# Optimization experiments

Measured on AMD Instinct MI355X. Metric: run time of the kernel, lower is better.

The kernel has to match this reference:

```python
import jax, jax.numpy as jnp
import numpy as np

N_NODES = 100000
N_EDGES = 1600000
DIM = 128


def setup_inputs() -> dict:
    key = jax.random.key(0)
    k_x, k_e, k_wm, k_bm, k_wu, k_bu = jax.random.split(key, 6)
    bound = 1.0 / np.sqrt(DIM)
    return {
        "x": jax.random.normal(k_x, (N_NODES, DIM), dtype=jnp.float32),
        "edge_index": jax.random.randint(k_e, (2, N_EDGES), 0, N_NODES, dtype=jnp.int64),
        "W_msg": jax.random.uniform(k_wm, (DIM, DIM), jnp.float32, -bound, bound),
        "b_msg": jax.random.uniform(k_bm, (DIM,), jnp.float32, -bound, bound),
        "W_upd": jax.random.uniform(k_wu, (DIM, DIM), jnp.float32, -bound, bound),
        "b_upd": jax.random.uniform(k_bu, (DIM,), jnp.float32, -bound, bound),
    }


def reference(x, edge_index, W_msg, b_msg, W_upd, b_upd):
    # message_net: Linear + ReLU on all nodes  [N, D]
    messages = jax.nn.relu(x @ W_msg.T + b_msg)
    src, dst = edge_index[0], edge_index[1]
    # gather by src, scatter-add by dst (index_add)  [N, D]
    aggregated = jax.ops.segment_sum(messages[src], dst, num_segments=x.shape[0])
    # update_net: Linear + ReLU, then residual
    updated = jax.nn.relu(aggregated @ W_upd.T + b_upd)
    return updated + x
```

## Files before the change

kernel.cpp:

```cpp
#include <hip/hip_runtime.h>
#include <hip/hip_bf16.h>

#define DIM 128
#define BNODES 64
#define CNODES 1024
#define NCMAX 128
#define NBMAX 2048
#define CCAP 20480
#define BCAP 2048
#define FB 16
#define CCHUNK 2048

typedef __attribute__((ext_vector_type(8))) short bf16x8;
typedef __attribute__((ext_vector_type(4))) float f32x4;

__device__ inline ushort f2bf(float f) {
    uint u = __float_as_uint(f);
    u += 0x7fffu + ((u >> 16) & 1u);
    return (ushort)(u >> 16);
}
__device__ inline uint pack2(float lo, float hi) {
    return (uint)f2bf(lo) | ((uint)f2bf(hi) << 16);
}

__device__ __forceinline__
void linear_body_bf16out(const float* in, const float* __restrict__ W,
                         const float* __restrict__ b, ushort* out,
                         int n_tiles, int bid, int nblocks, uint4* Wl)
{
    const int t = threadIdx.x;
    for (int q = t; q < 2048; q += 256) {
        const int j = q >> 4, c = q & 15;
        const float4 lo = ((const float4*)(W + j * 128 + c * 8))[0];
        const float4 hi = ((const float4*)(W + j * 128 + c * 8))[1];
        uint4 pk;
        pk.x = pack2(lo.x, lo.y); pk.y = pack2(lo.z, lo.w);
        pk.z = pack2(hi.x, hi.y); pk.w = pack2(hi.z, hi.w);
        Wl[j * 16 + (c ^ (j & 15))] = pk;
    }
    __syncthreads();

    const int lane = t & 63;
    const int lo4 = lane & 15;
    const int g   = lane >> 4;

    float bias[8];
    #pragma unroll
    for (int ct = 0; ct < 8; ++ct) bias[ct] = b[ct * 16 + lo4];

    const int wid = (bid * 256 + t) >> 6;
    const int nw  = (nblocks * 256) >> 6;

    for (int tile = wid; tile < n_tiles; tile += nw) {
        const int arow = tile * 16 + lo4;
        const float4* ap = (const float4*)(in + (size_t)arow * DIM + g * 32);
        float4 v[8];
        #pragma unroll
        for (int i = 0; i < 8; ++i) v[i] = ap[i];

        bf16x8 afrag[4];
        #pragma unroll
        for (int ks = 0; ks < 4; ++ks) {
            union { bf16x8 v8; uint u[4]; } a;
            a.u[0] = pack2(v[2*ks].x,   v[2*ks].y);
            a.u[1] = pack2(v[2*ks].z,   v[2*ks].w);
            a.u[2] = pack2(v[2*ks+1].x, v[2*ks+1].y);
            a.u[3] = pack2(v[2*ks+1].z, v[2*ks+1].w);
            afrag[ks] = a.v8;
        }

        f32x4 acc[8];
        #pragma unroll
        for (int ct = 0; ct < 8; ++ct)
            acc[ct] = (f32x4){bias[ct], bias[ct], bias[ct], bias[ct]};

        #pragma unroll
        for (int ks = 0; ks < 4; ++ks) {
            #pragma unroll
            for (int ct = 0; ct < 8; ++ct) {
                const int jrow = ct * 16 + lo4;
                const bf16x8 bfrag = *((const bf16x8*)&Wl[jrow * 16 + ((g * 4 + ks) ^ lo4)]);
                acc[ct] = __builtin_amdgcn_mfma_f32_16x16x32_bf16(afrag[ks], bfrag, acc[ct], 0, 0, 0);
            }
        }

        #pragma unroll
        for (int ct = 0; ct < 8; ++ct) {
            #pragma unroll
            for (int r = 0; r < 4; ++r) {
                const int orow = tile * 16 + g * 4 + r;
                const int ocol = ct * 16 + lo4;
                out[(size_t)orow * DIM + ocol] = f2bf(fmaxf(acc[ct][r], 0.f));
            }
        }
    }
}

__global__ __launch_bounds__(256, 2)
void lin1_coarse_kernel(const float* x, const float* __restrict__ Wm,
                        const float* __restrict__ bm, ushort* msg, int n_tiles,
                        const int* __restrict__ ei, int* __restrict__ ccur,
                        uint* __restrict__ cedges, int n_edges, int ncb, int cb)
{
    __shared__ uint4 Wl[128 * 16];

    const int bid = (int)blockIdx.x;
    bool coarse;
    int rid;
    if (bid < 2 * cb) { coarse = !(bid & 1); rid = bid >> 1; }
    else              { coarse = false;      rid = cb + (bid - 2 * cb); }

    if (coarse) {
        uint*   packedL = (uint*)Wl;
        ushort* regionL = (ushort*)(packedL + CCHUNK);
        int*    histC   = (int*)(regionL + CCHUNK);
        int*    startC  = histC + NCMAX;
        int*    gbaseC  = startC + NCMAX;
        int*    curC    = gbaseC + NCMAX;

        const int t = threadIdx.x;
        const int chunk = (n_edges + cb - 1) / cb;
        const int e0 = rid * chunk;
        const int e1 = min(e0 + chunk, n_edges);
        const int cnt = e1 - e0;

        if (t < NCMAX) histC[t] = 0;
        __syncthreads();
        for (int i = t; i < cnt; i += 256)
            atomicAdd(&histC[ei[n_edges + e0 + i] >> 10], 1);
        __syncthreads();
        if (t < NCMAX) startC[t] = histC[t];
        for (int off = 1; off < NCMAX; off <<= 1) {
            int add = 0;
            __syncthreads();
            if (t < NCMAX && t >= off) add = startC[t - off];
            __syncthreads();
            if (t < NCMAX) startC[t] += add;
        }
        __syncthreads();
        if (t < NCMAX) {
            const int excl = startC[t] - histC[t];
            startC[t] = excl;
            curC[t] = excl;
            gbaseC[t] = (t < ncb && histC[t]) ? atomicAdd(&ccur[t], histC[t]) : 0;
        }
        __syncthreads();
        for (int i = t; i < cnt; i += 256) {
            const int src = ei[e0 + i];
            const int dst = ei[n_edges + e0 + i];
            const int r = dst >> 10;
            const int pos = atomicAdd(&curC[r], 1);
            packedL[pos] = ((uint)src << 10) | (uint)(dst & 1023);
            regionL[pos] = (ushort)r;
        }
        __syncthreads();
        for (int i = t; i < cnt; i += 256) {
            const int r = regionL[i];
            const int off = gbaseC[r] + (i - startC[r]);
            if (off < CCAP)
                cedges[(size_t)r * CCAP + off] = packedL[i];
        }
    } else {
        linear_body_bf16out(x, Wm, bm, msg, n_tiles, rid,
                            (int)gridDim.x - cb, Wl);
    }
}

__global__ __launch_bounds__(256)
void fine_scatter_kernel(const int* __restrict__ ccnt, const uint* __restrict__ cedges,
                         int* __restrict__ gcur, uint* __restrict__ bedges, int ncb)
{
    __shared__ int histL[FB];
    __shared__ int curL[FB];
    const int t = threadIdx.x;
    const int c = blockIdx.x >> 3;
    const int s = blockIdx.x & 7;
    const int cnt = min(ccnt[c], CCAP);
    const int chunk = (cnt + 7) / 8;
    const int e0 = s * chunk;
    const int e1 = min(e0 + chunk, cnt);
    if (t < FB) histL[t] = 0;
    __syncthreads();
    const uint* ce = cedges + (size_t)c * CCAP;
    for (int i = e0 + t; i < e1; i += 256)
        atomicAdd(&histL[(ce[i] & 1023u) >> 6], 1);
    __syncthreads();
    if (t < FB)
        curL[t] = histL[t] ? atomicAdd(&gcur[c * FB + t], histL[t]) : 0;
    __syncthreads();
    for (int i = e0 + t; i < e1; i += 256) {
        const uint p = ce[i];
        const uint dl = p & 1023u;
        const int f = (int)(dl >> 6);
        const int pos = atomicAdd(&curL[f], 1);
        if (pos < BCAP)
            bedges[(size_t)(c * FB + f) * BCAP + pos] = ((p >> 10) << 6) | (dl & 63u);
    }
}

__global__ __launch_bounds__(512)
void bucket_gather_kernel(const uint* __restrict__ msg, const int* __restrict__ gcur,
                          const uint* __restrict__ bedges, uint* __restrict__ agg16,
                          int n_nodes)
{
    __shared__ int  srcL[BCAP];
    __shared__ int histL[BNODES];
    __shared__ int inclL[BNODES];
    __shared__ int cursL[BNODES];

    const int t = threadIdx.x;
    const int b = blockIdx.x;
    const int cnt = min(gcur[b], BCAP);
    const uint* be = bedges + (size_t)b * BCAP;

    if (t < BNODES) histL[t] = 0;
    __syncthreads();
    for (int i = t; i < cnt; i += 512)
        atomicAdd(&histL[be[i] & 63u], 1);
    __syncthreads();
    if (t < BNODES) inclL[t] = histL[t];
    for (int off = 1; off < BNODES; off <<= 1) {
        int add = 0;
        __syncthreads();
        if (t < BNODES && t >= off) add = inclL[t - off];
        __syncthreads();
        if (t < BNODES) inclL[t] += add;
    }
    __syncthreads();
    if (t < BNODES) cursL[t] = inclL[t] - histL[t];
    __syncthreads();
    for (int i = t; i < cnt; i += 512) {
        const uint p = be[i];
        const int pos = atomicAdd(&cursL[p & 63u], 1);
        srcL[pos] = (int)(p >> 6);
    }
    __syncthreads();

    const int lane = t & 63;
    const int w = t >> 6;
    for (int dl = w; dl < BNODES; dl += 8) {
        const int node = b * BNODES + dl;
        if (node >= n_nodes) break;
        const int e1 = inclL[dl];
        const int e0 = e1 - histL[dl];
        float a0 = 0.f, a1 = 0.f;
        int i = e0;
        for (; i + 8 <= e1; i += 8) {
            uint m[8];
            #pragma unroll
            for (int k = 0; k < 8; ++k)
                m[k] = msg[(size_t)srcL[i + k] * 64 + lane];
            #pragma unroll
            for (int k = 0; k < 8; ++k) {
                a0 += __uint_as_float(m[k] << 16);
                a1 += __uint_as_float(m[k] & 0xffff0000u);
            }
        }
        for (; i + 4 <= e1; i += 4) {
            uint m[4];
            #pragma unroll
            for (int k = 0; k < 4; ++k)
                m[k] = msg[(size_t)srcL[i + k] * 64 + lane];
            #pragma unroll
            for (int k = 0; k < 4; ++k) {
                a0 += __uint_as_float(m[k] << 16);
                a1 += __uint_as_float(m[k] & 0xffff0000u);
            }
        }
        for (; i < e1; ++i) {
            const uint m = msg[(size_t)srcL[i] * 64 + lane];
            a0 += __uint_as_float(m << 16);
            a1 += __uint_as_float(m & 0xffff0000u);
        }
        agg16[(size_t)node * 64 + lane] = pack2(a0, a1);
    }
}

__global__ __launch_bounds__(256, 2)
void lin2_a16_kernel(const uint4* __restrict__ agg16, const float* __restrict__ Wu,
                     const float* __restrict__ bu, const float* __restrict__ x,
                     float* __restrict__ out, int n_tiles)
{
    __shared__ uint4 Wl[128 * 16];
    const int t = threadIdx.x;
    for (int q = t; q < 2048; q += 256) {
        const int j = q >> 4, c = q & 15;
        const float4 lo = ((const float4*)(Wu + j * 128 + c * 8))[0];
        const float4 hi = ((const float4*)(Wu + j * 128 + c * 8))[1];
        uint4 pk;
        pk.x = pack2(lo.x, lo.y); pk.y = pack2(lo.z, lo.w);
        pk.z = pack2(hi.x, hi.y); pk.w = pack2(hi.z, hi.w);
        Wl[j * 16 + (c ^ (j & 15))] = pk;
    }
    __syncthreads();

    const int lane = t & 63;
    const int lo4 = lane & 15;
    const int g   = lane >> 4;

    float bias[8];
    #pragma unroll
    for (int ct = 0; ct < 8; ++ct) bias[ct] = bu[ct * 16 + lo4];

    const int wid = ((int)blockIdx.x * 256 + t) >> 6;
    const int nw  = ((int)gridDim.x * 256) >> 6;

    for (int tile = wid; tile < n_tiles; tile += nw) {
        const int arow = tile * 16 + lo4;
        bf16x8 afrag[4];
        #pragma unroll
        for (int ks = 0; ks < 4; ++ks) {
            const uint4 u = agg16[(size_t)arow * 16 + g * 4 + ks];
            afrag[ks] = *(const bf16x8*)&u;
        }

        f32x4 acc[8];
        #pragma unroll
        for (int ct = 0; ct < 8; ++ct)
            acc[ct] = (f32x4){bias[ct], bias[ct], bias[ct], bias[ct]};

        #pragma unroll
        for (int ks = 0; ks < 4; ++ks) {
            #pragma unroll
            for (int ct = 0; ct < 8; ++ct) {
                const int jrow = ct * 16 + lo4;
                const bf16x8 bfrag = *((const bf16x8*)&Wl[jrow * 16 + ((g * 4 + ks) ^ lo4)]);
                acc[ct] = __builtin_amdgcn_mfma_f32_16x16x32_bf16(afrag[ks], bfrag, acc[ct], 0, 0, 0);
            }
        }

        #pragma unroll
        for (int ct = 0; ct < 8; ++ct) {
            #pragma unroll
            for (int r = 0; r < 4; ++r) {
                const int orow = tile * 16 + g * 4 + r;
                const int ocol = ct * 16 + lo4;
                out[(size_t)orow * DIM + ocol] =
                    fmaxf(acc[ct][r], 0.f) + x[(size_t)orow * DIM + ocol];
            }
        }
    }
}

extern "C" void kernel_launch(void* const* d_in, const int* in_sizes, int n_in,
                              void* d_out, int out_size, void* d_ws, size_t ws_size,
                              hipStream_t stream)
{
    const float* x  = (const float*)d_in[0];
    const int*   ei = (const int*)d_in[1];
    const float* Wm = (const float*)d_in[2];
    const float* bm = (const float*)d_in[3];
    const float* Wu = (const float*)d_in[4];
    const float* bu = (const float*)d_in[5];

    const int N = in_sizes[0] / DIM;
    const int E = in_sizes[1] / 2;
    const int nb  = (N + BNODES - 1) / BNODES;
    const int ncb = (N + CNODES - 1) / CNODES;
    const int cb  = 782;

    char* ws = (char*)d_ws;
    ushort* msg = (ushort*)ws;
    size_t o = (size_t)N * DIM * sizeof(ushort);
    int* ccur = (int*)(ws + o); o += (size_t)NCMAX * 4;
    int* gcur = (int*)(ws + o); o += (size_t)NBMAX * 4;
    o = (o + 255) & ~(size_t)255;
    uint* cedges = (uint*)(ws + o); o += (size_t)ncb * CCAP * 4;
    o = (o + 255) & ~(size_t)255;
    uint* bedges = (uint*)(ws + o); o += (size_t)(nb + FB) * BCAP * 4;
    o = (o + 255) & ~(size_t)255;
    uint* agg16 = (uint*)(ws + o);
    const bool a16 = ws_size >= o + (size_t)N * 64 * 4;

    float* out = (float*)d_out;
    const int n_tiles = N / 16;

    hipMemsetAsync(ccur, 0, (size_t)(NCMAX + NBMAX) * 4, stream);

    lin1_coarse_kernel<<<2048, 256, 0, stream>>>(x, Wm, bm, msg, n_tiles,
                                                 ei, ccur, cedges, E, ncb, cb);

    fine_scatter_kernel<<<ncb * 8, 256, 0, stream>>>(ccur, cedges, gcur, bedges, ncb);

    bucket_gather_kernel<<<nb, 512, 0, stream>>>((const uint*)msg, gcur, bedges, agg16, N);

    lin2_a16_kernel<<<1024, 256, 0, stream>>>((const uint4*)agg16, Wu, bu, x, out, n_tiles);

    (void)a16;
}
```

Measured before the change: 140.1 us.

## Split fused lin1/coarse-sort kernel into two separate sequential launches

Undoes the horizontal fusion that interleaved the first linear layer and the coarse edge bucketing in one launch. The coarse sort now runs as its own kernel with statically sized shared memory, followed by a separate lin1 kernel with 1024 blocks. This removes the block-role branching and shared-memory aliasing, but gives up running the compute-bound GEMM concurrently with the atomic-heavy sort and adds one more launch.

```diff
diff --git a/kernel.cpp b/kernel.cpp
--- a/kernel.cpp
+++ b/kernel.cpp
@@ -23,11 +23,12 @@
     return (uint)f2bf(lo) | ((uint)f2bf(hi) << 16);
 }
 
-__device__ __forceinline__
-void linear_body_bf16out(const float* in, const float* __restrict__ W,
-                         const float* __restrict__ b, ushort* out,
-                         int n_tiles, int bid, int nblocks, uint4* Wl)
-{
+__global__ __launch_bounds__(256, 2)
+void lin1_kernel(const float* __restrict__ in, const float* __restrict__ W,
+                 const float* __restrict__ b, ushort* __restrict__ out, int n_tiles)
+{
+    __shared__ uint4 Wl[128 * 16];
+
     const int t = threadIdx.x;
     for (int q = t; q < 2048; q += 256) {
         const int j = q >> 4, c = q & 15;
@@ -48,8 +49,8 @@
     #pragma unroll
     for (int ct = 0; ct < 8; ++ct) bias[ct] = b[ct * 16 + lo4];
 
-    const int wid = (bid * 256 + t) >> 6;
-    const int nw  = (nblocks * 256) >> 6;
+    const int wid = ((int)blockIdx.x * 256 + t) >> 6;
+    const int nw  = ((int)gridDim.x * 256) >> 6;
 
     for (int tile = wid; tile < n_tiles; tile += nw) {
         const int arow = tile * 16 + lo4;
@@ -96,73 +97,59 @@
     }
 }
 
-__global__ __launch_bounds__(256, 2)
-void lin1_coarse_kernel(const float* x, const float* __restrict__ Wm,
-                        const float* __restrict__ bm, ushort* msg, int n_tiles,
-                        const int* __restrict__ ei, int* __restrict__ ccur,
+__global__ __launch_bounds__(256)
+void coarse_sort_kernel(const int* __restrict__ ei, int* __restrict__ ccur,
                         uint* __restrict__ cedges, int n_edges, int ncb, int cb)
 {
-    __shared__ uint4 Wl[128 * 16];
-
-    const int bid = (int)blockIdx.x;
-    bool coarse;
-    int rid;
-    if (bid < 2 * cb) { coarse = !(bid & 1); rid = bid >> 1; }
-    else              { coarse = false;      rid = cb + (bid - 2 * cb); }
-
-    if (coarse) {
-        uint*   packedL = (uint*)Wl;
-        ushort* regionL = (ushort*)(packedL + CCHUNK);
-        int*    histC   = (int*)(regionL + CCHUNK);
-        int*    startC  = histC + NCMAX;
-        int*    gbaseC  = startC + NCMAX;
-        int*    curC    = gbaseC + NCMAX;
-
-        const int t = threadIdx.x;
-        const int chunk = (n_edges + cb - 1) / cb;
-        const int e0 = rid * chunk;
-        const int e1 = min(e0 + chunk, n_edges);
-        const int cnt = e1 - e0;
-
-        if (t < NCMAX) histC[t] = 0;
+    __shared__ uint   packedL[CCHUNK];
+    __shared__ ushort regionL[CCHUNK];
+    __shared__ int histC[NCMAX];
+    __shared__ int startC[NCMAX];
+    __shared__ int gbaseC[NCMAX];
+    __shared__ int curC[NCMAX];
+
+    const int t = threadIdx.x;
+    const int rid = (int)blockIdx.x;
+    const int chunk = (n_edges + cb - 1) / cb;
+    const int e0 = rid * chunk;
+    const int e1 = min(e0 + chunk, n_edges);
+    const int cnt = e1 - e0;
+
+    if (t < NCMAX) histC[t] = 0;
+    __syncthreads();
+    for (int i = t; i < cnt; i += 256)
+        atomicAdd(&histC[ei[n_edges + e0 + i] >> 10], 1);
+    __syncthreads();
+    if (t < NCMAX) startC[t] = histC[t];
+    for (int off = 1; off < NCMAX; off <<= 1) {
+        int add = 0;
         __syncthreads();
-        for (int i = t; i < cnt; i += 256)
-            atomicAdd(&histC[ei[n_edges + e0 + i] >> 10], 1);
+        if (t < NCMAX && t >= off) add = startC[t - off];
         __syncthreads();
-        if (t < NCMAX) startC[t] = histC[t];
-        for (int off = 1; off < NCMAX; off <<= 1) {
-            int add = 0;
-            __syncthreads();
-            if (t < NCMAX && t >= off) add = startC[t - off];
-            __syncthreads();
-            if (t < NCMAX) startC[t] += add;
-        }
-        __syncthreads();
-        if (t < NCMAX) {
-            const int excl = startC[t] - histC[t];
-            startC[t] = excl;
-            curC[t] = excl;
-            gbaseC[t] = (t < ncb && histC[t]) ? atomicAdd(&ccur[t], histC[t]) : 0;
-        }
-        __syncthreads();
-        for (int i = t; i < cnt; i += 256) {
-            const int src = ei[e0 + i];
-            const int dst = ei[n_edges + e0 + i];
-            const int r = dst >> 10;
-            const int pos = atomicAdd(&curC[r], 1);
-            packedL[pos] = ((uint)src << 10) | (uint)(dst & 1023);
-            regionL[pos] = (ushort)r;
-        }
-        __syncthreads();
-        for (int i = t; i < cnt; i += 256) {
-            const int r = regionL[i];
-            const int off = gbaseC[r] + (i - startC[r]);
-            if (off < CCAP)
-                cedges[(size_t)r * CCAP + off] = packedL[i];
-        }
-    } else {
-        linear_body_bf16out(x, Wm, bm, msg, n_tiles, rid,
-                            (int)gridDim.x - cb, Wl);
+        if (t < NCMAX) startC[t] += add;
+    }
+    __syncthreads();
+    if (t < NCMAX) {
+        const int excl = startC[t] - histC[t];
+        startC[t] = excl;
+        curC[t] = excl;
+        gbaseC[t] = (t < ncb && histC[t]) ? atomicAdd(&ccur[t], histC[t]) : 0;
+    }
+    __syncthreads();
+    for (int i = t; i < cnt; i += 256) {
+        const int src = ei[e0 + i];
+        const int dst = ei[n_edges + e0 + i];
+        const int r = dst >> 10;
+        const int pos = atomicAdd(&curC[r], 1);
+        packedL[pos] = ((uint)src << 10) | (uint)(dst & 1023);
+        regionL[pos] = (ushort)r;
+    }
+    __syncthreads();
+    for (int i = t; i < cnt; i += 256) {
+        const int r = regionL[i];
+        const int off = gbaseC[r] + (i - startC[r]);
+        if (off < CCAP)
+            cedges[(size_t)r * CCAP + off] = packedL[i];
     }
 }
 
@@ -370,21 +357,19 @@
     uint* bedges = (uint*)(ws + o); o += (size_t)(nb + FB) * BCAP * 4;
     o = (o + 255) & ~(size_t)255;
     uint* agg16 = (uint*)(ws + o);
-    const bool a16 = ws_size >= o + (size_t)N * 64 * 4;
 
     float* out = (float*)d_out;
     const int n_tiles = N / 16;
 
     hipMemsetAsync(ccur, 0, (size_t)(NCMAX + NBMAX) * 4, stream);
 
-    lin1_coarse_kernel<<<2048, 256, 0, stream>>>(x, Wm, bm, msg, n_tiles,
-                                                 ei, ccur, cedges, E, ncb, cb);
+    coarse_sort_kernel<<<cb, 256, 0, stream>>>(ei, ccur, cedges, E, ncb, cb);
+
+    lin1_kernel<<<1024, 256, 0, stream>>>(x, Wm, bm, msg, n_tiles);
 
     fine_scatter_kernel<<<ncb * 8, 256, 0, stream>>>(ccur, cedges, gcur, bedges, ncb);
 
     bucket_gather_kernel<<<nb, 512, 0, stream>>>((const uint*)msg, gcur, bedges, agg16, N);
 
     lin2_a16_kernel<<<1024, 256, 0, stream>>>((const uint4*)agg16, Wu, bu, x, out, n_tiles);
-
-    (void)a16;
-}
+}
```

Measured after the change: 146.7 us. 4.7% more time.

## Split first linear across two kernels to overlap with coarse and fine scatter

Applied to the files above, without the earlier changes.

The first linear layer's tiles are split into two halves. The first half runs interleaved with the coarse edge bucketing, and the second half runs interleaved with the fine scatter, which was previously its own kernel. This hides the fine-scatter latency behind matmul work and balances blocks between phases. The cost is that each fused kernel must reload W into LDS. The fine-scatter blocks now also run at the heavier kernel's resource footprint, with 32KB of LDS.

```diff
diff --git a/kernel.cpp b/kernel.cpp
--- a/kernel.cpp
+++ b/kernel.cpp
@@ -24,9 +24,9 @@
 }
 
 __device__ __forceinline__
-void linear_body_bf16out(const float* in, const float* __restrict__ W,
-                         const float* __restrict__ b, ushort* out,
-                         int n_tiles, int bid, int nblocks, uint4* Wl)
+void lin1_body(const float* __restrict__ in, const float* __restrict__ W,
+               const float* __restrict__ b, ushort* __restrict__ out,
+               int tile0, int tcount, int bid, int nblocks, uint4* Wl)
 {
     const int t = threadIdx.x;
     for (int q = t; q < 2048; q += 256) {
@@ -50,8 +50,9 @@
 
     const int wid = (bid * 256 + t) >> 6;
     const int nw  = (nblocks * 256) >> 6;
-
-    for (int tile = wid; tile < n_tiles; tile += nw) {
+    const int tend = tile0 + tcount;
+
+    for (int tile = tile0 + wid; tile < tend; tile += nw) {
         const int arow = tile * 16 + lo4;
         const float4* ap = (const float4*)(in + (size_t)arow * DIM + g * 32);
         float4 v[8];
@@ -97,10 +98,11 @@
 }
 
 __global__ __launch_bounds__(256, 2)
-void lin1_coarse_kernel(const float* x, const float* __restrict__ Wm,
-                        const float* __restrict__ bm, ushort* msg, int n_tiles,
-                        const int* __restrict__ ei, int* __restrict__ ccur,
-                        uint* __restrict__ cedges, int n_edges, int ncb, int cb)
+void fusedA_kernel(const float* x, const float* __restrict__ Wm,
+                   const float* __restrict__ bm, ushort* msg,
+                   int tile0, int tcount, int lb,
+                   const int* __restrict__ ei, int* __restrict__ ccur,
+                   uint* __restrict__ cedges, int n_edges, int ncb, int cb)
 {
     __shared__ uint4 Wl[128 * 16];
 
@@ -161,40 +163,55 @@
                 cedges[(size_t)r * CCAP + off] = packedL[i];
         }
     } else {
-        linear_body_bf16out(x, Wm, bm, msg, n_tiles, rid,
-                            (int)gridDim.x - cb, Wl);
-    }
-}
-
-__global__ __launch_bounds__(256)
-void fine_scatter_kernel(const int* __restrict__ ccnt, const uint* __restrict__ cedges,
-                         int* __restrict__ gcur, uint* __restrict__ bedges, int ncb)
-{
+        lin1_body(x, Wm, bm, msg, tile0, tcount, rid, lb, Wl);
+    }
+}
+
+__global__ __launch_bounds__(256, 2)
+void fusedB_kernel(const float* x, const float* __restrict__ Wm,
+                   const float* __restrict__ bm, ushort* msg,
+                   int tile0, int tcount, int lb,
+                   const int* __restrict__ ccnt, const uint* __restrict__ cedges,
+                   int* __restrict__ gcur, uint* __restrict__ bedges,
+                   int ncb, int fb)
+{
+    __shared__ uint4 Wl[128 * 16];
     __shared__ int histL[FB];
     __shared__ int curL[FB];
-    const int t = threadIdx.x;
-    const int c = blockIdx.x >> 3;
-    const int s = blockIdx.x & 7;
-    const int cnt = min(ccnt[c], CCAP);
-    const int chunk = (cnt + 7) / 8;
-    const int e0 = s * chunk;
-    const int e1 = min(e0 + chunk, cnt);
-    if (t < FB) histL[t] = 0;
-    __syncthreads();
-    const uint* ce = cedges + (size_t)c * CCAP;
-    for (int i = e0 + t; i < e1; i += 256)
-        atomicAdd(&histL[(ce[i] & 1023u) >> 6], 1);
-    __syncthreads();
-    if (t < FB)
-        curL[t] = histL[t] ? atomicAdd(&gcur[c * FB + t], histL[t]) : 0;
-    __syncthreads();
-    for (int i = e0 + t; i < e1; i += 256) {
-        const uint p = ce[i];
-        const uint dl = p & 1023u;
-        const int f = (int)(dl >> 6);
-        const int pos = atomicAdd(&curL[f], 1);
-        if (pos < BCAP)
-            bedges[(size_t)(c * FB + f) * BCAP + pos] = ((p >> 10) << 6) | (dl & 63u);
+
+    const int bid = (int)blockIdx.x;
+    bool fine;
+    int rid;
+    if (bid < 2 * fb) { fine = !(bid & 1); rid = bid >> 1; }
+    else              { fine = false;      rid = fb + (bid - 2 * fb); }
+
+    if (fine) {
+        const int t = threadIdx.x;
+        const int c = rid >> 3;
+        const int s = rid & 7;
+        const int cnt = min(ccnt[c], CCAP);
+        const int chunk = (cnt + 7) / 8;
+        const int e0 = s * chunk;
+        const int e1 = min(e0 + chunk, cnt);
+        if (t < FB) histL[t] = 0;
+        __syncthreads();
+        const uint* ce = cedges + (size_t)c * CCAP;
+        for (int i = e0 + t; i < e1; i += 256)
+            atomicAdd(&histL[(ce[i] & 1023u) >> 6], 1);
+        __syncthreads();
+        if (t < FB)
+            curL[t] = histL[t] ? atomicAdd(&gcur[c * FB + t], histL[t]) : 0;
+        __syncthreads();
+        for (int i = e0 + t; i < e1; i += 256) {
+            const uint p = ce[i];
+            const uint dl = p & 1023u;
+            const int f = (int)(dl >> 6);
+            const int pos = atomicAdd(&curL[f], 1);
+            if (pos < BCAP)
+                bedges[(size_t)(c * FB + f) * BCAP + pos] = ((p >> 10) << 6) | (dl & 63u);
+        }
+    } else {
+        lin1_body(x, Wm, bm, msg, tile0, tcount, rid, lb, Wl);
     }
 }
 
@@ -358,6 +375,8 @@
     const int nb  = (N + BNODES - 1) / BNODES;
     const int ncb = (N + CNODES - 1) / CNODES;
     const int cb  = 782;
+    const int fb  = ncb * 8;
+    const int lb  = 1024;
 
     char* ws = (char*)d_ws;
     ushort* msg = (ushort*)ws;
@@ -370,21 +389,20 @@
     uint* bedges = (uint*)(ws + o); o += (size_t)(nb + FB) * BCAP * 4;
     o = (o + 255) & ~(size_t)255;
     uint* agg16 = (uint*)(ws + o);
-    const bool a16 = ws_size >= o + (size_t)N * 64 * 4;
 
     float* out = (float*)d_out;
     const int n_tiles = N / 16;
+    const int half = n_tiles / 2;
 
     hipMemsetAsync(ccur, 0, (size_t)(NCMAX + NBMAX) * 4, stream);
 
-    lin1_coarse_kernel<<<2048, 256, 0, stream>>>(x, Wm, bm, msg, n_tiles,
-                                                 ei, ccur, cedges, E, ncb, cb);
-
-    fine_scatter_kernel<<<ncb * 8, 256, 0, stream>>>(ccur, cedges, gcur, bedges, ncb);
+    fusedA_kernel<<<2 * cb + (lb - cb), 256, 0, stream>>>(
+        x, Wm, bm, msg, 0, half, lb, ei, ccur, cedges, E, ncb, cb);
+
+    fusedB_kernel<<<2 * fb + (lb - fb), 256, 0, stream>>>(
+        x, Wm, bm, msg, half, n_tiles - half, lb, ccur, cedges, gcur, bedges, ncb, fb);
 
     bucket_gather_kernel<<<nb, 512, 0, stream>>>((const uint*)msg, gcur, bedges, agg16, N);
 
     lin2_a16_kernel<<<1024, 256, 0, stream>>>((const uint4*)agg16, Wu, bu, x, out, n_tiles);
-
-    (void)a16;
-}
+}
```

Result: slower. 152.4 us (+8.8%).
